# Performance work log

Measured on AMD Instinct MI355X. Metric: run time of the kernel, lower is better.

## Reference

```python
import jax, jax.numpy as jnp
from jax import lax
import numpy as np

PRE_NMS_TOPN = 2000
POST_NMS_TOPN = 300
NMS_IOU_THRESHOLD = 0.7
EPS = 1e-8


def setup_inputs() -> dict:
    key = jax.random.key(0)
    k1, k2 = jax.random.split(key, 2)
    B, H, W, A = 64, 100, 100, 9
    # small-magnitude deltas so exp(dh/dw) stays sane, as real RPN outputs do
    rpn_bbox_deltas = jax.random.normal(k1, (B, H, W, A * 4), dtype=jnp.float32) * 0.1
    rpn_labels = jax.random.uniform(k2, (B, H, W, A), dtype=jnp.float32)
    # grid anchors, normalized coords, 3 scales x 3 ratios = 9 per position
    ys = (jnp.arange(H, dtype=jnp.float32) + 0.5) / H
    xs = (jnp.arange(W, dtype=jnp.float32) + 0.5) / W
    scales = jnp.array([0.1, 0.2, 0.4], dtype=jnp.float32)
    ratios = jnp.array([0.5, 1.0, 2.0], dtype=jnp.float32)
    hh = (scales[:, None] * jnp.sqrt(ratios)[None, :]).reshape(-1)  # [9]
    ww = (scales[:, None] / jnp.sqrt(ratios)[None, :]).reshape(-1)  # [9]
    cy, cx = jnp.meshgrid(ys, xs, indexing="ij")  # [H,W]
    cy, cx = cy[..., None], cx[..., None]         # [H,W,1]
    anchors = jnp.stack(
        [cy - hh / 2, cx - ww / 2, cy + hh / 2, cx + ww / 2], axis=-1
    ).reshape(-1, 4)  # [H*W*9, 4] = [90000, 4]
    return {"rpn_bbox_deltas": rpn_bbox_deltas, "rpn_labels": rpn_labels, "anchors": anchors}


def _decode_deltas(anchors, deltas):
    # anchors [N,4] (y1,x1,y2,x2), deltas [B,N,4] (dy,dx,dh,dw)
    anc_h = anchors[:, 2] - anchors[:, 0]
    anc_w = anchors[:, 3] - anchors[:, 1]
    anc_cy = anchors[:, 0] + 0.5 * anc_h
    anc_cx = anchors[:, 1] + 0.5 * anc_w
    h = jnp.exp(deltas[..., 2]) * anc_h
    w = jnp.exp(deltas[..., 3]) * anc_w
    cy = deltas[..., 0] * anc_h + anc_cy
    cx = deltas[..., 1] * anc_w + anc_cx
    y1 = cy - 0.5 * h
    x1 = cx - 0.5 * w
    return jnp.stack([y1, x1, y1 + h, x1 + w], axis=-1)  # [B,N,4]


def _nms_single(boxes):
    # boxes [PRE,4] already sorted by score descending; greedy hard NMS
    n = boxes.shape[0]
    area = jnp.maximum(boxes[:, 2] - boxes[:, 0], 0.0) * jnp.maximum(boxes[:, 3] - boxes[:, 1], 0.0)
    idx = jnp.arange(n)

    def body(i, keep):
        b = boxes[i]
        yy1 = jnp.maximum(b[0], boxes[:, 0])
        xx1 = jnp.maximum(b[1], boxes[:, 1])
        yy2 = jnp.minimum(b[2], boxes[:, 2])
        xx2 = jnp.minimum(b[3], boxes[:, 3])
        inter = jnp.maximum(yy2 - yy1, 0.0) * jnp.maximum(xx2 - xx1, 0.0)
        iou = inter / (area[i] + area - inter + EPS)
        suppress = (iou > NMS_IOU_THRESHOLD) & (idx > i) & keep[i]
        return keep & ~suppress

    keep = lax.fori_loop(0, n, body, jnp.ones((n,), dtype=bool))
    # compact kept boxes (score order) into fixed [POST,4], zero-padded
    pos = jnp.where(keep, jnp.cumsum(keep) - 1, POST_NMS_TOPN)
    pos = jnp.minimum(pos, POST_NMS_TOPN)
    out = jnp.zeros((POST_NMS_TOPN + 1, 4), dtype=boxes.dtype).at[pos].set(boxes)[:POST_NMS_TOPN]
    return jnp.clip(out, 0.0, 1.0)  # clip_boxes=True in tf combined NMS


def reference(rpn_bbox_deltas, rpn_labels, anchors):
    B = rpn_bbox_deltas.shape[0]
    N = anchors.shape[0]
    deltas = rpn_bbox_deltas.reshape(B, N, 4)
    labels = rpn_labels.reshape(B, N)
    boxes = _decode_deltas(anchors, deltas)             # [B,N,4]
    _, pre_idx = lax.top_k(labels, PRE_NMS_TOPN)        # [B,PRE] sorted desc
    pre_boxes = jnp.take_along_axis(boxes, pre_idx[..., None], axis=1)  # [B,PRE,4]
    roi_bboxes = jax.vmap(_nms_single)(pre_boxes)       # [B,POST,4]
    return lax.stop_gradient(roi_bboxes)
```

## Files before the change

kernel.cpp:

```cpp
#include <hip/hip_runtime.h>
#include <stdint.h>


#define PRE 2000
#define POST 300
#define TILE 512
#define IOU_THR 0.7f
#define EPSV 1e-8f
#define SORTN 2048
#define NBINS 2048
#define DESTCAP 4096
#define CANDCAP 512
#define CONS 1984
#define SL 16
#define KBUF 768

typedef unsigned long long u64;

__device__ __forceinline__ uint32_t flip_f32(uint32_t b) {
    return b ^ ((uint32_t)((int32_t)b >> 31) | 0x80000000u);
}

__device__ __forceinline__ int bin_of(float s) {
    int bn = (int)(s * 2048.0f);
    return min(max(bn, 0), NBINS - 1);
}

__device__ __forceinline__ u64 make_key(float s, int idx, int bn) {
    uint32_t ub = flip_f32(__float_as_uint(s));
    return ((u64)ub << 32) | ((uint32_t)bn << 20) |
           (uint32_t)(0xFFFFF - idx);
}

__device__ __forceinline__ bool iou_gt(const float4& bi, float ai,
                                       const float4& bj, float aj) {
    float yy1 = fmaxf(bi.x, bj.x);
    float xx1 = fmaxf(bi.y, bj.y);
    float yy2 = fminf(bi.z, bj.z);
    float xx2 = fminf(bi.w, bj.w);
    float inter = fmaxf(yy2 - yy1, 0.f) * fmaxf(xx2 - xx1, 0.f);
    float iou = inter / (ai + aj - inter + EPSV);
    return iou > IOU_THR;
}

__device__ __forceinline__ float area_of(const float4& bx) {
    return fmaxf(bx.z - bx.x, 0.f) * fmaxf(bx.w - bx.y, 0.f);
}

__device__ __forceinline__ float4 decode_key(u64 key, const float4* dl,
                                             const float4* anchors, int N) {
    uint32_t idx = 0xFFFFFu - (uint32_t)(key & 0xFFFFFull);
    if (idx >= (uint32_t)N) return make_float4(0.f, 0.f, 0.f, 0.f);
    float4 d  = dl[idx];
    float4 an = anchors[idx];
    float ah  = an.z - an.x;
    float aw  = an.w - an.y;
    float acy = an.x + 0.5f * ah;
    float acx = an.y + 0.5f * aw;
    float h   = expf(d.z) * ah;
    float w   = expf(d.w) * aw;
    float cy  = d.x * ah + acy;
    float cx  = d.y * aw + acx;
    float y1  = cy - 0.5f * h;
    float x1  = cx - 0.5f * w;
    return make_float4(y1, x1, y1 + h, x1 + w);
}

__device__ __forceinline__ u64 cs_keep(u64 v, u64 pv, int i, int j, int k) {
    bool lower   = ((i & j) == 0);
    bool desc    = ((i & k) == 0);
    bool keepmax = (desc == lower);
    u64 mx = v > pv ? v : pv;
    u64 mn = v > pv ? pv : v;
    return keepmax ? mx : mn;
}

__global__ __launch_bounds__(256) void k1_gather(
    const float4* __restrict__ score4,
    u64* __restrict__ g_pairs,
    int* __restrict__ g_scnt,
    uint32_t* __restrict__ g_shist,
    int N)
{
    const int blk = blockIdx.x;
    const int b   = blk / SL;
    const int s   = blk % SL;
    const int tid = threadIdx.x;
    const int lane = tid & 63;
    const int F4PB = N >> 2;
    const int F4PS = (F4PB + SL - 1) / SL;

    __shared__ u64 keybuf[KBUF];
    __shared__ u64 binbuf[KBUF];
    __shared__ uint32_t hist64[64];
    __shared__ int base64[64];
    __shared__ uint32_t cur64[64];
    __shared__ int kcnt;

    if (tid < 64) { hist64[tid] = 0u; cur64[tid] = 0u; }
    if (tid == 0) kcnt = 0;
    __syncthreads();

    const float4* src = score4 + (size_t)b * F4PB;
    const int n0 = s * F4PS, n1 = min(n0 + F4PS, F4PB);
    for (int n = n0 + tid; n < n1; n += 256) {
        float4 v = src[n];
        float sv[4] = {v.x, v.y, v.z, v.w};
#pragma unroll
        for (int c = 0; c < 4; ++c) {
            int bn = bin_of(sv[c]);
            if (bn >= CONS) {
                int q = atomicAdd(&kcnt, 1);
                if (q < KBUF) keybuf[q] = make_key(sv[c], 4 * n + c, bn);
            }
        }
    }
    __syncthreads();

    const int raw = kcnt;
    const int lc  = min(raw, KBUF);

    for (int i = tid; i < lc; i += 256) {
        int b64 = (int)((keybuf[i] >> 20) & 0xFFFu) - CONS;
        atomicAdd(&hist64[b64], 1u);
    }
    __syncthreads();

    if (tid < 64) {
        int h = (int)hist64[lane];
        int ssum = h;
#pragma unroll
        for (int off = 1; off < 64; off <<= 1) {
            int t = __shfl_down(ssum, off, 64);
            if (lane + off < 64) ssum += t;
        }
        base64[lane] = ssum - h;
    }
    __syncthreads();

    for (int i = tid; i < lc; i += 256) {
        u64 key = keybuf[i];
        int b64 = (int)((key >> 20) & 0xFFFu) - CONS;
        int p = (int)atomicAdd(&cur64[b64], 1u);
        binbuf[base64[b64] + p] = key;
    }
    __syncthreads();

    if (tid == 0) g_scnt[b * SL + s] = raw;
    if (tid < 64) g_shist[((size_t)b * SL + s) * 64 + tid] = hist64[tid];
    u64* gp = g_pairs + ((size_t)b * SL + s) * KBUF;
    for (int i = tid; i < lc; i += 256) gp[i] = binbuf[i];
}

__global__ __launch_bounds__(1024) void k2_sort(
    const float4* __restrict__ score4,
    const u64*  __restrict__ g_pairs,
    const int*  __restrict__ g_scnt,
    const uint32_t* __restrict__ g_shist,
    u64* __restrict__ g_sorted,
    int N)
{
    const int b    = blockIdx.x;
    const int tid  = threadIdx.x;
    const int lane = tid & 63;
    const int wv   = tid >> 6;

    __shared__ u64 dest[DESTCAP];
    __shared__ uint32_t hist2048[NBINS];
    __shared__ u64 cand[CANDCAP];
    __shared__ uint32_t shist[SL][64];
    __shared__ int srcb[SL][64];
    __shared__ int sbase[SL][64];
    __shared__ int tot64[64];
    __shared__ int segbase64[64];
    __shared__ uint32_t wtot[16];
    __shared__ int sh_flag, sh_total, sh_bsel, sh_tprime, sh_cnt, sh_nc;
    __shared__ uint32_t sh_pivot;

    const int F4PB = N >> 2;

    shist[tid >> 6][tid & 63] = g_shist[(size_t)b * SL * 64 + tid];
    if (tid == 0) {
        int f = 0;
#pragma unroll
        for (int s = 0; s < SL; ++s)
            if (g_scnt[b * SL + s] > KBUF) f = 1;
        sh_flag = f;
    }
    __syncthreads();

    if (tid < 64) {
        int acc = 0;
#pragma unroll
        for (int s = 0; s < SL; ++s) acc += (int)shist[s][tid];
        tot64[tid] = acc;
        if (acc > 128) sh_flag = 1;
    }
    {
        int h = (int)shist[wv][lane];
        int ssum = h;
#pragma unroll
        for (int off = 1; off < 64; off <<= 1) {
            int t = __shfl_down(ssum, off, 64);
            if (lane + off < 64) ssum += t;
        }
        srcb[wv][lane] = ssum - h;
    }
    __syncthreads();

    if (tid < 64) {
        int t0 = tot64[lane];
        int ssum = t0;
#pragma unroll
        for (int off = 1; off < 64; off <<= 1) {
            int t = __shfl_down(ssum, off, 64);
            if (lane + off < 64) ssum += t;
        }
        segbase64[lane] = ssum - t0;
        if (lane == 0) sh_total = ssum;
    }
    __syncthreads();
    const int total = sh_total;
    if (tid == 0 && (total < PRE || total > DESTCAP)) sh_flag = 1;
    {
        int s   = tid >> 6;
        int b64 = tid & 63;
        int pre = 0;
        for (int s2 = 0; s2 < s; ++s2) pre += (int)shist[s2][b64];
        sbase[s][b64] = segbase64[b64] + pre;
    }
    __syncthreads();
    const bool flag = (sh_flag != 0);

    if (!flag) {
        const int cs = min(g_scnt[b * SL + wv], KBUF);
        const u64* gp = g_pairs + ((size_t)b * SL + wv) * KBUF;
        for (int i = lane; i < cs; i += 64) {
            u64 key = gp[i];
            int b64 = (int)((key >> 20) & 0xFFFu) - CONS;
            dest[sbase[wv][b64] + (i - srcb[wv][b64])] = key;
        }
        __syncthreads();
        for (int sgi = wv; sgi < 64; sgi += 16) {
            int n = tot64[sgi];
            if (n <= 0) continue;
            int base = segbase64[sgi];
            if (n <= 64) {
                u64 e = (lane < n) ? dest[base + lane] : 0ull;
#pragma unroll
                for (int k = 2; k <= 64; k <<= 1)
                    for (int j = k >> 1; j > 0; j >>= 1)
                        e = cs_keep(e, __shfl_xor(e, j, 64), lane, j, k);
                if (lane < n) dest[base + lane] = e;
            } else {
                u64 e0 = (lane < n) ? dest[base + lane] : 0ull;
                u64 e1 = (lane + 64 < n) ? dest[base + lane + 64] : 0ull;
#pragma unroll
                for (int k = 2; k <= 128; k <<= 1) {
                    for (int j = k >> 1; j > 0; j >>= 1) {
                        if (j == 64) {
                            u64 a = e0, c = e1;
                            e0 = cs_keep(a, c, lane, 64, k);
                            e1 = cs_keep(c, a, lane + 64, 64, k);
                        } else {
                            e0 = cs_keep(e0, __shfl_xor(e0, j, 64), lane, j, k);
                            e1 = cs_keep(e1, __shfl_xor(e1, j, 64), lane + 64, j, k);
                        }
                    }
                }
                if (lane < n) dest[base + lane] = e0;
                if (lane + 64 < n) dest[base + lane + 64] = e1;
            }
        }
        __syncthreads();
        g_sorted[(size_t)b * SORTN + tid]        = dest[tid];
        g_sorted[(size_t)b * SORTN + tid + 1024] = dest[tid + 1024];
    } else {
        hist2048[tid] = 0u; hist2048[tid + 1024] = 0u;
        if (tid == 0) { sh_cnt = 0; sh_nc = 0; }
        __syncthreads();
        const float4* src = score4 + (size_t)b * F4PB;
        for (int n = tid; n < F4PB; n += 1024) {
            float4 v = src[n];
            atomicAdd(&hist2048[bin_of(v.x)], 1u);
            atomicAdd(&hist2048[bin_of(v.y)], 1u);
            atomicAdd(&hist2048[bin_of(v.z)], 1u);
            atomicAdd(&hist2048[bin_of(v.w)], 1u);
        }
        __syncthreads();
        {
            const int i0 = wv * 128 + lane;
            const int i1 = i0 + 64;
            int h0 = (int)hist2048[i0];
            int h1 = (int)hist2048[i1];
            int s0 = h0, s1 = h1;
#pragma unroll
            for (int off = 1; off < 64; off <<= 1) {
                int t0 = __shfl_down(s0, off, 64);
                int t1 = __shfl_down(s1, off, 64);
                if (lane + off < 64) { s0 += t0; s1 += t1; }
            }
            int sum_h1 = __shfl(s1, 0, 64);
            if (lane == 0) wtot[wv] = (uint32_t)(__shfl(s0, 0, 64) + sum_h1);
            __syncthreads();
            int offtot = 0;
            for (int w2 = wv + 1; w2 < 16; ++w2) offtot += (int)wtot[w2];
            int S0 = s0 + sum_h1 + offtot;
            int S1 = s1 + offtot;
            if (S0 >= PRE && S0 - h0 < PRE) { sh_bsel = i0; sh_tprime = PRE - (S0 - h0); }
            if (S1 >= PRE && S1 - h1 < PRE) { sh_bsel = i1; sh_tprime = PRE - (S1 - h1); }
        }
        __syncthreads();
        const int bsel   = sh_bsel;
        const int tprime = sh_tprime;
        for (int n = tid; n < F4PB; n += 1024) {
            float4 v = src[n];
            float sv[4] = {v.x, v.y, v.z, v.w};
#pragma unroll
            for (int c = 0; c < 4; ++c) {
                int bn = bin_of(sv[c]);
                if (bn >= bsel) {
                    u64 key = make_key(sv[c], 4 * n + c, bn);
                    if (bn > bsel) {
                        int q = atomicAdd(&sh_cnt, 1);
                        if (q < SORTN) dest[q] = key;
                    } else {
                        int t = atomicAdd(&sh_nc, 1);
                        if (t < CANDCAP) cand[t] = key;
                    }
                }
            }
        }
        __syncthreads();
        const int nc = min(sh_nc, CANDCAP);
        for (int i = tid; i < nc; i += 1024) {
            uint32_t vi = (uint32_t)(cand[i] >> 32);
            int g = 0, e = 0;
            for (int j = 0; j < nc; ++j) {
                uint32_t vj = (uint32_t)(cand[j] >> 32);
                g += (vj > vi);
                e += (vj == vi);
            }
            if (g < tprime && g + e >= tprime) sh_pivot = vi;
        }
        __syncthreads();
        const uint32_t pivot = sh_pivot;
        for (int i = tid; i < nc; i += 1024) {
            uint32_t vi = (uint32_t)(cand[i] >> 32);
            if (vi >= pivot) {
                int q = atomicAdd(&sh_cnt, 1);
                if (q < SORTN) dest[q] = cand[i];
            }
        }
        __syncthreads();
        const int tt = min(sh_cnt, SORTN);
        for (int q = tt + tid; q < SORTN; q += 1024) dest[q] = 0ull;
        __syncthreads();
        {
            const int i0 = wv * 128 + lane;
            const int i1 = i0 + 64;
            u64 e0 = dest[i0];
            u64 e1 = dest[i1];
            for (int k = 2; k <= SORTN; k <<= 1) {
                for (int j = k >> 1; j > 0; j >>= 1) {
                    if (j >= 128) {
                        dest[i0] = e0;
                        dest[i1] = e1;
                        __syncthreads();
                        u64 p0 = dest[i0 ^ j];
                        u64 p1 = dest[i1 ^ j];
                        __syncthreads();
                        e0 = cs_keep(e0, p0, i0, j, k);
                        e1 = cs_keep(e1, p1, i1, j, k);
                    } else if (j == 64) {
                        u64 a = e0, c = e1;
                        e0 = cs_keep(a, c, i0, 64, k);
                        e1 = cs_keep(c, a, i1, 64, k);
                    } else {
                        e0 = cs_keep(e0, __shfl_xor(e0, j, 64), i0, j, k);
                        e1 = cs_keep(e1, __shfl_xor(e1, j, 64), i1, j, k);
                    }
                }
            }
            g_sorted[(size_t)b * SORTN + i0] = e0;
            g_sorted[(size_t)b * SORTN + i1] = e1;
        }
    }
}

__global__ __launch_bounds__(256) void k4_supmat(
    const float4* __restrict__ deltas,
    const float4* __restrict__ anchors,
    const u64*  __restrict__ g_sorted,
    float4* __restrict__ g_boxes,
    uint32_t* __restrict__ g_supmat,
    uint32_t* __restrict__ g_supT,
    int N)
{
    const int b   = blockIdx.x >> 4;
    const int s   = blockIdx.x & 15;
    const int tid = threadIdx.x;

    __shared__ float4 box[TILE];

    const float4* dl = deltas + (size_t)b * N;
#pragma unroll
    for (int k = 0; k < 2; ++k) {
        int r = tid + k * 256;
        box[r] = decode_key(g_sorted[(size_t)b * SORTN + r], dl, anchors, N);
    }
    __syncthreads();

    if (s == 0) {
#pragma unroll
        for (int k = 0; k < 2; ++k) {
            int r = tid + k * 256;
            g_boxes[(size_t)b * TILE + r] = box[r];
        }
    }

    const int rbase = s * 32;
#pragma unroll
    for (int k = 0; k < 2; ++k) {
        int idx = tid + k * 256;
        int row = rbase + (idx & 31);
        int w   = idx >> 5;
        int jbase = w << 5;
        float4 bi = box[row];
        float  ai = area_of(bi);
        uint32_t bits = 0u;
        if (jbase + 31 > row) {
#pragma unroll
            for (int c = 0; c < 32; ++c) {
                int j = jbase + c;
                float4 bj = box[j];
                float  aj = area_of(bj);
                bool gt = (j > row) & iou_gt(bi, ai, bj, aj);
                bits |= ((uint32_t)gt) << c;
            }
        }
        g_supmat[((size_t)b * TILE + row) * 16 + w] = bits;
    }

    if (s < 8 && tid < 128) {
        int q  = s;
        int j  = tid >> 1;
        int w2 = tid & 1;
        int C  = q * 64 + j;
        float4 bc = box[C];
        float  ac = area_of(bc);
        uint32_t bits = 0u;
#pragma unroll
        for (int c = 0; c < 32; ++c) {
            int R = q * 64 + w2 * 32 + c;
            float4 br = box[R];
            float  ar = area_of(br);
            bool gt = (R < C) & iou_gt(br, ar, bc, ac);
            bits |= ((uint32_t)gt) << c;
        }
        g_supT[((size_t)b * TILE + C) * 2 + w2] = bits;
    }
}

__global__ __launch_bounds__(64) void k5_sweep(
    const uint32_t* __restrict__ g_supmat,
    const u64*    __restrict__ g_supT64,
    const u64*    __restrict__ g_sorted,
    const float4* __restrict__ deltas,
    const float4* __restrict__ anchors,
    const float4* __restrict__ g_boxes,
    float4* __restrict__ out,
    int N)
{
    const int b    = blockIdx.x;
    const int lane = threadIdx.x;

    __shared__ uint32_t kept[POST];
    __shared__ u64 sh_keepbits[TILE / 64];
    __shared__ int sh_kc;
    __shared__ float4 fbox[PRE];
    __shared__ float  farea[PRE];
    __shared__ uint32_t fmask[(PRE - TILE + 31) / 32];

    const u64* tdbase = g_supT64 + (size_t)b * TILE;

    uint32_t removedw = 0u;
    int kc = 0, nq = 0;
    u64 cw_cur = tdbase[lane];
    for (int q = 0; q < TILE / 64; ++q) {
        u64 cw_next = (q < TILE / 64 - 1) ? tdbase[(q + 1) * 64 + lane] : 0ull;
        const int cbase = q << 6;
        uint32_t rlo = (uint32_t)__builtin_amdgcn_readlane((int)removedw, 2 * q);
        uint32_t rhi = (uint32_t)__builtin_amdgcn_readlane((int)removedw, 2 * q + 1);
        u64 avail = ~(((u64)rhi << 32) | rlo);
        u64 K = 0ull;
        while (avail) {
            int i = __ffsll((long long)avail) - 1;
            K |= (1ull << i);
            u64 supp = __ballot(((cw_cur >> i) & 1ull) != 0ull);
            avail &= ~(supp | (1ull << i));
        }
        if (lane == 0) sh_keepbits[q] = K;
        kc += __popcll(K);
        nq = q + 1;
        if (kc >= POST) break;
        if (K) {
            const int w = lane & 15;
            const int g = lane >> 4;
            const uint32_t* gs =
                g_supmat + ((size_t)b * TILE + cbase + g * 16) * 16 + w;
            uint32_t acc = 0u;
#pragma unroll
            for (int r = 0; r < 16; ++r) {
                uint32_t v = gs[(size_t)r * 16];
                uint32_t m = (uint32_t)0 - (uint32_t)((K >> (g * 16 + r)) & 1ull);
                acc |= (v & m);
            }
            acc |= (uint32_t)__shfl_xor((int)acc, 16, 64);
            acc |= (uint32_t)__shfl_xor((int)acc, 32, 64);
            if (lane < 16) removedw |= acc;
        }
        cw_cur = cw_next;
    }
    {
        int base = 0;
        for (int q = 0; q < nq; ++q) {
            u64 kbq = sh_keepbits[q];
            int pos = base + __popcll(kbq & ((1ull << lane) - 1));
            if (((kbq >> lane) & 1ull) && pos < POST)
                kept[pos] = (uint32_t)(q * 64 + lane);
            base += __popcll(kbq);
        }
        if (lane == 0) sh_kc = min(kc, POST);
    }
    __syncthreads();
    int kcf = sh_kc;
    const bool fellback = (kcf < POST);

    if (fellback) {
        const float4* dl = deltas + (size_t)b * N;
        for (int r = lane; r < PRE; r += 64) {
            float4 bx = decode_key(g_sorted[(size_t)b * SORTN + r], dl,
                                   anchors, N);
            fbox[r]  = bx;
            farea[r] = area_of(bx);
        }
        for (int w = lane; w < (PRE - TILE + 31) / 32; w += 64) fmask[w] = 0u;
        __syncthreads();
        for (int j = TILE + lane; j < PRE; j += 64) {
            float4 bj = fbox[j];
            float  aj = farea[j];
            bool supd = false;
            for (int k = 0; k < kcf; ++k) {
                int i = (int)kept[k];
                if (iou_gt(fbox[i], farea[i], bj, aj)) { supd = true; break; }
            }
            if (supd) atomicOr(&fmask[(j - TILE) >> 5], 1u << ((j - TILE) & 31));
        }
        __syncthreads();
        int i = TILE;
        while (i < PRE && kcf < POST) {
            while (i < PRE && ((fmask[(i - TILE) >> 5] >> ((i - TILE) & 31)) & 1u)) ++i;
            if (i >= PRE) break;
            if (lane == 0) kept[kcf] = (uint32_t)i;
            ++kcf;
            if (kcf >= POST) break;
            float4 bi = fbox[i];
            float  ai = farea[i];
            for (int j = i + 1 + lane; j < PRE; j += 64) {
                if (iou_gt(bi, ai, fbox[j], farea[j]))
                    atomicOr(&fmask[(j - TILE) >> 5], 1u << ((j - TILE) & 31));
            }
            ++i;
            __syncthreads();
        }
    }
    __syncthreads();

    float4* ob = out + (size_t)b * POST;
    for (int r = lane; r < POST; r += 64) {
        float4 o = make_float4(0.f, 0.f, 0.f, 0.f);
        if (r < kcf) {
            int ki = (int)kept[r];
            float4 bx = fellback ? fbox[ki]
                                 : g_boxes[(size_t)b * TILE + ki];
            o.x = fminf(fmaxf(bx.x, 0.f), 1.f);
            o.y = fminf(fmaxf(bx.y, 0.f), 1.f);
            o.z = fminf(fmaxf(bx.z, 0.f), 1.f);
            o.w = fminf(fmaxf(bx.w, 0.f), 1.f);
        }
        ob[r] = o;
    }
}

extern "C" void kernel_launch(void* const* d_in, const int* in_sizes, int n_in,
                              void* d_out, int out_size, void* d_ws, size_t ws_size,
                              hipStream_t stream) {
    const float4* deltas  = (const float4*)d_in[0];
    const float*  labels  = (const float*)d_in[1];
    const float4* anchors = (const float4*)d_in[2];
    const float4* score4  = (const float4*)labels;
    float4*       outp    = (float4*)d_out;
    const int N = in_sizes[2] / 4;
    const int B = in_sizes[1] / N;

    char* ws = (char*)d_ws;
    const size_t SZ_BOXES  = (size_t)B * TILE * 16;
    const size_t SZ_PAIRS  = (size_t)B * SL * KBUF * 8;
    const size_t SZ_SORTED = (size_t)B * SORTN * 8;
    const size_t SZ_SUPMAT = (size_t)B * TILE * 16 * 4;
    const size_t SZ_SUPT   = (size_t)B * TILE * 8;
    const size_t SZ_SHIST  = (size_t)B * SL * 64 * 4;
    float4*   g_boxes  = (float4*)ws;
    u64*      g_pairs  = (u64*)(ws + SZ_BOXES);
    u64*      g_sorted = (u64*)(ws + SZ_BOXES + SZ_PAIRS);
    uint32_t* g_supmat = (uint32_t*)(ws + SZ_BOXES + SZ_PAIRS + SZ_SORTED);
    uint32_t* g_supT   = (uint32_t*)(ws + SZ_BOXES + SZ_PAIRS + SZ_SORTED + SZ_SUPMAT);
    uint32_t* g_shist  = (uint32_t*)(ws + SZ_BOXES + SZ_PAIRS + SZ_SORTED + SZ_SUPMAT + SZ_SUPT);
    int*      g_scnt   = (int*)((char*)g_shist + SZ_SHIST);

    k1_gather<<<B * SL, 256, 0, stream>>>(score4, g_pairs, g_scnt, g_shist, N);
    k2_sort<<<B, 1024, 0, stream>>>(score4, g_pairs, g_scnt, g_shist,
                                    g_sorted, N);
    k4_supmat<<<B * 16, 256, 0, stream>>>(deltas, anchors, g_sorted,
                                          g_boxes, g_supmat, g_supT, N);
    k5_sweep<<<B, 64, 0, stream>>>(g_supmat, (const u64*)g_supT, g_sorted,
                                   deltas, anchors, g_boxes, outp, N);
}
```

Baseline: 75.68 us.

## Fuse suppression-matrix and sweep kernels via last-block-done atomic counter

Merges the separate sweep kernel into the suppression-matrix kernel. Each of the 16 blocks per batch increments a per-batch global counter, and the last block to finish runs the greedy sweep using its own shared-memory boxes instead of a global box copy. This removes one kernel launch, the launch gap between the two kernels, and the global box buffer write and read. In exchange the fallback path now keeps its boxes in global scratch (aliased onto the pairs buffer) rather than shared memory, which makes that path slower. The counters are reset inside the first kernel.

```diff
diff --git a/kernel.cpp b/kernel.cpp
--- a/kernel.cpp
+++ b/kernel.cpp
@@ -80,6 +80,7 @@
     u64* __restrict__ g_pairs,
     int* __restrict__ g_scnt,
     uint32_t* __restrict__ g_shist,
+    int* __restrict__ g_cnt,
     int N)
 {
     const int blk = blockIdx.x;
@@ -89,6 +90,7 @@
     const int lane = tid & 63;
     const int F4PB = N >> 2;
     const int F4PS = (F4PB + SL - 1) / SL;
+    const int B    = (int)gridDim.x / SL;
 
     __shared__ u64 keybuf[KBUF];
     __shared__ u64 binbuf[KBUF];
@@ -96,6 +98,8 @@
     __shared__ int base64[64];
     __shared__ uint32_t cur64[64];
     __shared__ int kcnt;
+
+    if (tid == 0 && blk < B) g_cnt[blk] = 0;
 
     if (tid < 64) { hist64[tid] = 0u; cur64[tid] = 0u; }
     if (tid == 0) kcnt = 0;
@@ -388,20 +392,27 @@
     }
 }
 
-__global__ __launch_bounds__(256) void k4_supmat(
+__global__ __launch_bounds__(256) void k4_supmat_sweep(
     const float4* __restrict__ deltas,
     const float4* __restrict__ anchors,
     const u64*  __restrict__ g_sorted,
-    float4* __restrict__ g_boxes,
     uint32_t* __restrict__ g_supmat,
     uint32_t* __restrict__ g_supT,
+    int*      __restrict__ g_cnt,
+    float4*   __restrict__ fb_scratch,
+    float4*   __restrict__ out,
     int N)
 {
-    const int b   = blockIdx.x >> 4;
-    const int s   = blockIdx.x & 15;
-    const int tid = threadIdx.x;
+    const int b    = blockIdx.x >> 4;
+    const int s    = blockIdx.x & 15;
+    const int tid  = threadIdx.x;
+    const int lane = tid & 63;
 
     __shared__ float4 box[TILE];
+    __shared__ uint32_t kept[POST];
+    __shared__ u64 sh_keepbits[TILE / 64];
+    __shared__ uint32_t fmask[(PRE - TILE + 31) / 32];
+    __shared__ int sh_last;
 
     const float4* dl = deltas + (size_t)b * N;
 #pragma unroll
@@ -410,14 +421,6 @@
         box[r] = decode_key(g_sorted[(size_t)b * SORTN + r], dl, anchors, N);
     }
     __syncthreads();
-
-    if (s == 0) {
-#pragma unroll
-        for (int k = 0; k < 2; ++k) {
-            int r = tid + k * 256;
-            g_boxes[(size_t)b * TILE + r] = box[r];
-        }
-    }
 
     const int rbase = s * 32;
 #pragma unroll
@@ -460,136 +463,124 @@
         }
         g_supT[((size_t)b * TILE + C) * 2 + w2] = bits;
     }
-}
-
-__global__ __launch_bounds__(64) void k5_sweep(
-    const uint32_t* __restrict__ g_supmat,
-    const u64*    __restrict__ g_supT64,
-    const u64*    __restrict__ g_sorted,
-    const float4* __restrict__ deltas,
-    const float4* __restrict__ anchors,
-    const float4* __restrict__ g_boxes,
-    float4* __restrict__ out,
-    int N)
-{
-    const int b    = blockIdx.x;
-    const int lane = threadIdx.x;
-
-    __shared__ uint32_t kept[POST];
-    __shared__ u64 sh_keepbits[TILE / 64];
-    __shared__ int sh_kc;
-    __shared__ float4 fbox[PRE];
-    __shared__ float  farea[PRE];
-    __shared__ uint32_t fmask[(PRE - TILE + 31) / 32];
-
-    const u64* tdbase = g_supT64 + (size_t)b * TILE;
-
-    uint32_t removedw = 0u;
-    int kc = 0, nq = 0;
-    u64 cw_cur = tdbase[lane];
-    for (int q = 0; q < TILE / 64; ++q) {
-        u64 cw_next = (q < TILE / 64 - 1) ? tdbase[(q + 1) * 64 + lane] : 0ull;
-        const int cbase = q << 6;
-        uint32_t rlo = (uint32_t)__builtin_amdgcn_readlane((int)removedw, 2 * q);
-        uint32_t rhi = (uint32_t)__builtin_amdgcn_readlane((int)removedw, 2 * q + 1);
-        u64 avail = ~(((u64)rhi << 32) | rlo);
-        u64 K = 0ull;
-        while (avail) {
-            int i = __ffsll((long long)avail) - 1;
-            K |= (1ull << i);
-            u64 supp = __ballot(((cw_cur >> i) & 1ull) != 0ull);
-            avail &= ~(supp | (1ull << i));
-        }
-        if (lane == 0) sh_keepbits[q] = K;
-        kc += __popcll(K);
-        nq = q + 1;
-        if (kc >= POST) break;
-        if (K) {
-            const int w = lane & 15;
-            const int g = lane >> 4;
-            const uint32_t* gs =
-                g_supmat + ((size_t)b * TILE + cbase + g * 16) * 16 + w;
-            uint32_t acc = 0u;
-#pragma unroll
-            for (int r = 0; r < 16; ++r) {
-                uint32_t v = gs[(size_t)r * 16];
-                uint32_t m = (uint32_t)0 - (uint32_t)((K >> (g * 16 + r)) & 1ull);
-                acc |= (v & m);
-            }
-            acc |= (uint32_t)__shfl_xor((int)acc, 16, 64);
-            acc |= (uint32_t)__shfl_xor((int)acc, 32, 64);
-            if (lane < 16) removedw |= acc;
-        }
-        cw_cur = cw_next;
-    }
+
+    __threadfence();
+    if (tid == 0) {
+        int old = __hip_atomic_fetch_add(&g_cnt[b], 1, __ATOMIC_ACQ_REL,
+                                         __HIP_MEMORY_SCOPE_AGENT);
+        sh_last = (old == SL - 1);
+    }
+    __syncthreads();
+    if (!sh_last) return;
+    __threadfence();
+
+    if (tid >= 64) return;
     {
-        int base = 0;
-        for (int q = 0; q < nq; ++q) {
-            u64 kbq = sh_keepbits[q];
-            int pos = base + __popcll(kbq & ((1ull << lane) - 1));
-            if (((kbq >> lane) & 1ull) && pos < POST)
-                kept[pos] = (uint32_t)(q * 64 + lane);
-            base += __popcll(kbq);
-        }
-        if (lane == 0) sh_kc = min(kc, POST);
-    }
-    __syncthreads();
-    int kcf = sh_kc;
-    const bool fellback = (kcf < POST);
-
-    if (fellback) {
-        const float4* dl = deltas + (size_t)b * N;
-        for (int r = lane; r < PRE; r += 64) {
-            float4 bx = decode_key(g_sorted[(size_t)b * SORTN + r], dl,
+        const u64* tdbase = (const u64*)g_supT + (size_t)b * TILE;
+
+        uint32_t removedw = 0u;
+        int kc = 0, nq = 0;
+        u64 cw_cur = tdbase[lane];
+        for (int q = 0; q < TILE / 64; ++q) {
+            u64 cw_next = (q < TILE / 64 - 1) ? tdbase[(q + 1) * 64 + lane] : 0ull;
+            const int cbase = q << 6;
+            uint32_t rlo = (uint32_t)__builtin_amdgcn_readlane((int)removedw, 2 * q);
+            uint32_t rhi = (uint32_t)__builtin_amdgcn_readlane((int)removedw, 2 * q + 1);
+            u64 avail = ~(((u64)rhi << 32) | rlo);
+            u64 K = 0ull;
+            while (avail) {
+                int i = __ffsll((long long)avail) - 1;
+                K |= (1ull << i);
+                u64 supp = __ballot(((cw_cur >> i) & 1ull) != 0ull);
+                avail &= ~(supp | (1ull << i));
+            }
+            if (lane == 0) sh_keepbits[q] = K;
+            kc += __popcll(K);
+            nq = q + 1;
+            if (kc >= POST) break;
+            if (K) {
+                const int w = lane & 15;
+                const int g = lane >> 4;
+                const uint32_t* gs =
+                    g_supmat + ((size_t)b * TILE + cbase + g * 16) * 16 + w;
+                uint32_t acc = 0u;
+#pragma unroll
+                for (int r = 0; r < 16; ++r) {
+                    uint32_t v = gs[(size_t)r * 16];
+                    uint32_t m = (uint32_t)0 - (uint32_t)((K >> (g * 16 + r)) & 1ull);
+                    acc |= (v & m);
+                }
+                acc |= (uint32_t)__shfl_xor((int)acc, 16, 64);
+                acc |= (uint32_t)__shfl_xor((int)acc, 32, 64);
+                if (lane < 16) removedw |= acc;
+            }
+            cw_cur = cw_next;
+        }
+        {
+            int base = 0;
+            for (int q = 0; q < nq; ++q) {
+                u64 kbq = sh_keepbits[q];
+                int pos = base + __popcll(kbq & ((1ull << lane) - 1));
+                if (((kbq >> lane) & 1ull) && pos < POST)
+                    kept[pos] = (uint32_t)(q * 64 + lane);
+                base += __popcll(kbq);
+            }
+        }
+        int kcf = min(kc, POST);
+        const bool fellback = (kcf < POST);
+
+        float4* fb = fb_scratch + (size_t)b * PRE;
+        if (fellback) {
+            for (int r = lane; r < PRE; r += 64)
+                fb[r] = decode_key(g_sorted[(size_t)b * SORTN + r], dl,
                                    anchors, N);
-            fbox[r]  = bx;
-            farea[r] = area_of(bx);
-        }
-        for (int w = lane; w < (PRE - TILE + 31) / 32; w += 64) fmask[w] = 0u;
-        __syncthreads();
-        for (int j = TILE + lane; j < PRE; j += 64) {
-            float4 bj = fbox[j];
-            float  aj = farea[j];
-            bool supd = false;
-            for (int k = 0; k < kcf; ++k) {
-                int i = (int)kept[k];
-                if (iou_gt(fbox[i], farea[i], bj, aj)) { supd = true; break; }
-            }
-            if (supd) atomicOr(&fmask[(j - TILE) >> 5], 1u << ((j - TILE) & 31));
-        }
-        __syncthreads();
-        int i = TILE;
-        while (i < PRE && kcf < POST) {
-            while (i < PRE && ((fmask[(i - TILE) >> 5] >> ((i - TILE) & 31)) & 1u)) ++i;
-            if (i >= PRE) break;
-            if (lane == 0) kept[kcf] = (uint32_t)i;
-            ++kcf;
-            if (kcf >= POST) break;
-            float4 bi = fbox[i];
-            float  ai = farea[i];
-            for (int j = i + 1 + lane; j < PRE; j += 64) {
-                if (iou_gt(bi, ai, fbox[j], farea[j]))
+            for (int w = lane; w < (PRE - TILE + 31) / 32; w += 64)
+                fmask[w] = 0u;
+            for (int j = TILE + lane; j < PRE; j += 64) {
+                float4 bj = fb[j];
+                float  aj = area_of(bj);
+                bool supd = false;
+                for (int k = 0; k < kcf; ++k) {
+                    int i = (int)kept[k];
+                    float4 bi = fb[i];
+                    if (iou_gt(bi, area_of(bi), bj, aj)) { supd = true; break; }
+                }
+                if (supd)
                     atomicOr(&fmask[(j - TILE) >> 5], 1u << ((j - TILE) & 31));
             }
-            ++i;
-            __syncthreads();
-        }
-    }
-    __syncthreads();
-
-    float4* ob = out + (size_t)b * POST;
-    for (int r = lane; r < POST; r += 64) {
-        float4 o = make_float4(0.f, 0.f, 0.f, 0.f);
-        if (r < kcf) {
-            int ki = (int)kept[r];
-            float4 bx = fellback ? fbox[ki]
-                                 : g_boxes[(size_t)b * TILE + ki];
-            o.x = fminf(fmaxf(bx.x, 0.f), 1.f);
-            o.y = fminf(fmaxf(bx.y, 0.f), 1.f);
-            o.z = fminf(fmaxf(bx.z, 0.f), 1.f);
-            o.w = fminf(fmaxf(bx.w, 0.f), 1.f);
-        }
-        ob[r] = o;
+            int i = TILE;
+            while (i < PRE && kcf < POST) {
+                while (i < PRE &&
+                       ((fmask[(i - TILE) >> 5] >> ((i - TILE) & 31)) & 1u)) ++i;
+                if (i >= PRE) break;
+                if (lane == 0) kept[kcf] = (uint32_t)i;
+                ++kcf;
+                if (kcf >= POST) break;
+                float4 bi = fb[i];
+                float  ai = area_of(bi);
+                for (int j = i + 1 + lane; j < PRE; j += 64) {
+                    float4 bj = fb[j];
+                    if (iou_gt(bi, ai, bj, area_of(bj)))
+                        atomicOr(&fmask[(j - TILE) >> 5],
+                                 1u << ((j - TILE) & 31));
+                }
+                ++i;
+            }
+        }
+
+        float4* ob = out + (size_t)b * POST;
+        for (int r = lane; r < POST; r += 64) {
+            float4 o = make_float4(0.f, 0.f, 0.f, 0.f);
+            if (r < kcf) {
+                int ki = (int)kept[r];
+                float4 bx = fellback ? fb[ki] : box[ki];
+                o.x = fminf(fmaxf(bx.x, 0.f), 1.f);
+                o.y = fminf(fmaxf(bx.y, 0.f), 1.f);
+                o.z = fminf(fmaxf(bx.z, 0.f), 1.f);
+                o.w = fminf(fmaxf(bx.w, 0.f), 1.f);
+            }
+            ob[r] = o;
+        }
     }
 }
 
@@ -605,25 +596,26 @@
     const int B = in_sizes[1] / N;
 
     char* ws = (char*)d_ws;
-    const size_t SZ_BOXES  = (size_t)B * TILE * 16;
     const size_t SZ_PAIRS  = (size_t)B * SL * KBUF * 8;
     const size_t SZ_SORTED = (size_t)B * SORTN * 8;
     const size_t SZ_SUPMAT = (size_t)B * TILE * 16 * 4;
     const size_t SZ_SUPT   = (size_t)B * TILE * 8;
     const size_t SZ_SHIST  = (size_t)B * SL * 64 * 4;
-    float4*   g_boxes  = (float4*)ws;
-    u64*      g_pairs  = (u64*)(ws + SZ_BOXES);
-    u64*      g_sorted = (u64*)(ws + SZ_BOXES + SZ_PAIRS);
-    uint32_t* g_supmat = (uint32_t*)(ws + SZ_BOXES + SZ_PAIRS + SZ_SORTED);
-    uint32_t* g_supT   = (uint32_t*)(ws + SZ_BOXES + SZ_PAIRS + SZ_SORTED + SZ_SUPMAT);
-    uint32_t* g_shist  = (uint32_t*)(ws + SZ_BOXES + SZ_PAIRS + SZ_SORTED + SZ_SUPMAT + SZ_SUPT);
+    const size_t SZ_SCNT   = (size_t)B * SL * 4;
+    u64*      g_pairs  = (u64*)ws;
+    u64*      g_sorted = (u64*)(ws + SZ_PAIRS);
+    uint32_t* g_supmat = (uint32_t*)(ws + SZ_PAIRS + SZ_SORTED);
+    uint32_t* g_supT   = (uint32_t*)(ws + SZ_PAIRS + SZ_SORTED + SZ_SUPMAT);
+    uint32_t* g_shist  = (uint32_t*)(ws + SZ_PAIRS + SZ_SORTED + SZ_SUPMAT + SZ_SUPT);
     int*      g_scnt   = (int*)((char*)g_shist + SZ_SHIST);
-
-    k1_gather<<<B * SL, 256, 0, stream>>>(score4, g_pairs, g_scnt, g_shist, N);
+    int*      g_cnt    = (int*)((char*)g_scnt + SZ_SCNT);
+    float4*   fb       = (float4*)g_pairs;
+
+    k1_gather<<<B * SL, 256, 0, stream>>>(score4, g_pairs, g_scnt, g_shist,
+                                          g_cnt, N);
     k2_sort<<<B, 1024, 0, stream>>>(score4, g_pairs, g_scnt, g_shist,
                                     g_sorted, N);
-    k4_supmat<<<B * 16, 256, 0, stream>>>(deltas, anchors, g_sorted,
-                                          g_boxes, g_supmat, g_supT, N);
-    k5_sweep<<<B, 64, 0, stream>>>(g_supmat, (const u64*)g_supT, g_sorted,
-                                   deltas, anchors, g_boxes, outp, N);
-}
+    k4_supmat_sweep<<<B * 16, 256, 0, stream>>>(deltas, anchors, g_sorted,
+                                                g_supmat, g_supT, g_cnt,
+                                                fb, outp, N);
+}
```

Result: slower. 214.0 us (+182.7%).
